# Kernel optimization log

Measured on AMD Instinct MI355X. Metric: run time of the kernel, lower is better.

Reference implementation:

```python
import jax, jax.numpy as jnp
import numpy as np
import math

B_, V_, D_, N_, H_, W_ = 4, 8, 64, 16, 32, 32
V_LIST = [0.0, 45.0, 90.0, 135.0, 180.0, 225.0, 270.0, 315.0]
GROUPS = 4
EPS = 1e-5


def _make_sample_coords():
    # Replicates F.affine_grid(align_corners=False) for fixed rotation matrices,
    # then maps normalized grid coords to input pixel coords as grid_sample does.
    xs = (np.arange(W_) + 0.5) * 2.0 / W_ - 1.0
    ys = (np.arange(H_) + 0.5) * 2.0 / H_ - 1.0
    X, Y = np.meshgrid(xs, ys)  # (H, W)
    ix_list, iy_list = [], []
    for w in V_LIST:
        a = math.radians(-w)
        c, s = math.cos(a), math.sin(a)
        gx = c * X - s * Y  # theta = [[c,-s,0],[s,c,0]]
        gy = s * X + c * Y
        ix_list.append((gx + 1.0) * W_ / 2.0 - 0.5)
        iy_list.append((gy + 1.0) * H_ / 2.0 - 0.5)
    return (jnp.asarray(np.stack(ix_list), jnp.float32),
            jnp.asarray(np.stack(iy_list), jnp.float32))

IX, IY = _make_sample_coords()  # each (V, H, W)


def _bilinear(sv, iy, ix):
    # sv: (B, D, N, H, W); iy, ix: (H, W) float sampling coords (pixel space)
    x0 = jnp.floor(ix)
    y0 = jnp.floor(iy)
    wx1 = ix - x0
    wy1 = iy - y0

    def corner(yc, xc, wgt):
        m = (yc >= 0) & (yc < H_) & (xc >= 0) & (xc < W_)  # zeros padding
        yi = jnp.clip(yc, 0, H_ - 1).astype(jnp.int32)
        xi = jnp.clip(xc, 0, W_ - 1).astype(jnp.int32)
        return sv[..., yi, xi] * jnp.where(m, wgt, 0.0)

    return (corner(y0, x0, (1.0 - wy1) * (1.0 - wx1))
            + corner(y0, x0 + 1.0, (1.0 - wy1) * wx1)
            + corner(y0 + 1.0, x0, wy1 * (1.0 - wx1))
            + corner(y0 + 1.0, x0 + 1.0, wy1 * wx1))

# vmap over the velocity axis V of s_prev and the per-velocity grids
_transport = jax.vmap(_bilinear, in_axes=(1, 0, 0), out_axes=1)


def _conv(x, w, b=None):
    y = jax.lax.conv_general_dilated(x, w, (1, 1), 'SAME',
                                     dimension_numbers=('NCHW', 'OIHW', 'NCHW'))
    if b is not None:
        y = y + b[None, :, None, None]
    return y


def _group_norm(x, w, b):
    Bn, D, H, W = x.shape
    xg = x.reshape(Bn, GROUPS, D // GROUPS, H, W)
    mu = xg.mean(axis=(2, 3, 4), keepdims=True)
    var = xg.var(axis=(2, 3, 4), keepdims=True)
    xn = ((xg - mu) * jax.lax.rsqrt(var + EPS)).reshape(Bn, D, H, W)
    return xn * w[None, :, None, None] + b[None, :, None, None]


def setup_inputs() -> dict:
    key = jax.random.key(0)
    ks = jax.random.split(key, 5)
    return {
        "u_t": jax.random.normal(ks[0], (B_, D_, H_, W_), jnp.float32),
        "s_prev": jax.random.normal(ks[1], (B_, V_, D_, N_, H_, W_), jnp.float32) * 0.1,
        "gn_w": jnp.ones((D_,), jnp.float32),
        "gn_b": jnp.zeros((D_,), jnp.float32),
        "conv_delta_w": jax.random.normal(ks[2], (D_, D_, 3, 3), jnp.float32) * 0.02,
        "conv_delta_b": jnp.zeros((D_,), jnp.float32),
        "conv_B_w": jax.random.normal(ks[3], (N_, D_, 3, 3), jnp.float32) * 0.02,
        "conv_C_w": jax.random.normal(ks[4], (N_, D_, 3, 3), jnp.float32) * 0.02,
        "log_A_real": jnp.full((D_, N_), math.log(0.5), jnp.float32),
        "D_param": jnp.ones((D_,), jnp.float32),
        "dt_bias": jnp.float32(math.log(math.e - 1.0)),
    }


def reference(u_t, s_prev, gn_w, gn_b, conv_delta_w, conv_delta_b,
              conv_B_w, conv_C_w, log_A_real, D_param, dt_bias):
    u_norm = _group_norm(u_t, gn_w, gn_b)
    delta = jax.nn.softplus(_conv(u_norm, conv_delta_w, conv_delta_b) + dt_bias)
    delta = jnp.clip(delta, 1e-4, 5.0)                               # (B,D,H,W)
    B_val = _conv(u_norm, conv_B_w)                                  # (B,N,H,W)
    C_val = _conv(u_norm, conv_C_w)                                  # (B,N,H,W)
    A = -jnp.exp(log_A_real)                                         # (D,N)
    A_bar = jnp.exp(delta[:, :, None] * A[None, :, :, None, None])   # (B,D,N,H,W)
    B_bar = delta[:, :, None] * B_val[:, None]                       # (B,D,N,H,W)
    s_trans = _transport(s_prev, IY, IX)                             # (B,V,D,N,H,W)
    s_new = A_bar[:, None] * s_trans + B_bar[:, None] * u_t[:, None, :, None]
    y_state = jnp.einsum('bvdnhw,bnhw->bvdhw', s_new, C_val)
    y_new = y_state + u_t[:, None] * D_param[None, None, :, None, None]
    return (y_new, s_new)
```

## Files before the change

kernel.cpp:

```cpp
#include <hip/hip_runtime.h>
#include <cmath>

#define FSQ 0.70710678118654752440f
__constant__ float CTAB[8] = {1.f,  FSQ, 0.f, -FSQ, -1.f, -FSQ, 0.f, FSQ};
__constant__ float STAB[8] = {0.f, -FSQ, -1.f, -FSQ,  0.f,  FSQ, 1.f, FSQ};

__global__ __launch_bounds__(256) void gn_kernel(const float* __restrict__ u,
                                                 const float* __restrict__ gw,
                                                 const float* __restrict__ gb,
                                                 float* __restrict__ up)
{
    int blk = blockIdx.x;
    int b = blk >> 2, g = blk & 3;
    int t = threadIdx.x;
    const float* src = u + ((size_t)(b * 64 + g * 16) << 10);
    float sum = 0.f, sq = 0.f;
    #pragma unroll
    for (int r = 0; r < 64; ++r) {
        float v = src[t + (r << 8)];
        sum += v; sq += v * v;
    }
    __shared__ float red[256], red2[256];
    red[t] = sum; red2[t] = sq;
    __syncthreads();
    for (int ofs = 128; ofs > 0; ofs >>= 1) {
        if (t < ofs) { red[t] += red[t + ofs]; red2[t] += red2[t + ofs]; }
        __syncthreads();
    }
    float mu  = red[0] * (1.f / 16384.f);
    float var = red2[0] * (1.f / 16384.f) - mu * mu;
    float rs  = rsqrtf(var + 1e-5f);

    float* pb = up + (size_t)(b * 64 + g * 16) * 1156;
    for (int k = t; k < 16 * 132; k += 256) {
        int pl = k / 132, c = k % 132;
        int idx;
        if (c < 34)       idx = c;
        else if (c < 68)  idx = 33 * 34 + (c - 34);
        else if (c < 100) idx = (c - 68 + 1) * 34;
        else              idx = (c - 100 + 1) * 34 + 33;
        pb[pl * 1156 + idx] = 0.f;
    }
    for (int r = 0; r < 64; ++r) {
        int idx = t + (r << 8);
        int ch = idx >> 10, rem = idx & 1023;
        int y = rem >> 5, x = rem & 31;
        float val = (src[idx] - mu) * rs * gw[g * 16 + ch] + gb[g * 16 + ch];
        pb[ch * 1156 + (y + 1) * 34 + (x + 1)] = val;
    }
}

__global__ __launch_bounds__(256) void conv_kernel(const float* __restrict__ up,
                                                   const float* __restrict__ wd,
                                                   const float* __restrict__ bd,
                                                   const float* __restrict__ wB,
                                                   const float* __restrict__ wC,
                                                   const float* __restrict__ dtb,
                                                   float* __restrict__ delta,
                                                   float* __restrict__ Bv,
                                                   float* __restrict__ Cv)
{
    __shared__ float sin_[64 * 204];
    __shared__ float red[256];
    int blk = blockIdx.x;
    int strip = blk & 7;
    int o = (blk >> 3) & 127; o = o % 96;
    o = ((blk >> 3) - (blk / 768) * 96);
    int b = blk / 768;
    int h0 = strip * 4;
    int t = threadIdx.x;

    const float* plane = up + (size_t)b * 73984;
    for (int idx = t; idx < 13056; idx += 256) {
        int ci = idx / 204;
        int rem = idx - ci * 204;
        sin_[idx] = plane[ci * 1156 + h0 * 34 + rem];
    }
    __syncthreads();

    const float* wsel;
    if (o < 64)      wsel = wd + (size_t)o * 576;
    else if (o < 80) wsel = wB + (size_t)(o - 64) * 576;
    else             wsel = wC + (size_t)(o - 80) * 576;

    int half = t >> 7;
    int px = t & 127;
    int r = px >> 5, c = px & 31;
    const float* base = sin_ + r * 34 + c;

    float acc = 0.f;
    int ci0 = half * 32;
    for (int ci = ci0; ci < ci0 + 32; ++ci) {
        const float* pp = base + ci * 204;
        const float* wp = wsel + ci * 9;
        #pragma unroll
        for (int dy = 0; dy < 3; ++dy)
            #pragma unroll
            for (int dx = 0; dx < 3; ++dx)
                acc += pp[dy * 34 + dx] * wp[dy * 3 + dx];
    }
    red[t] = acc;
    __syncthreads();
    if (t < 128) {
        float a = red[t] + red[t + 128];
        int pidx = (h0 + r) * 32 + c;
        if (o < 64) {
            float x = a + bd[o] + dtb[0];
            float sp = (x > 20.f) ? x : log1pf(expf(x));
            sp = fminf(fmaxf(sp, 1e-4f), 5.f);
            delta[((size_t)(b * 64 + o) << 10) + pidx] = sp;
        } else if (o < 80) {
            Bv[((size_t)(b * 16 + o - 64) << 10) + pidx] = a;
        } else {
            Cv[((size_t)(b * 16 + o - 80) << 10) + pidx] = a;
        }
    }
}

__global__ __launch_bounds__(256) void fused_state_kernel(
    const float* __restrict__ s_prev, const float* __restrict__ u_t,
    const float* __restrict__ delta, const float* __restrict__ Bv,
    const float* __restrict__ Cv, const float* __restrict__ logA,
    const float* __restrict__ Dp, float* __restrict__ y_out,
    float* __restrict__ s_out)
{
    __shared__ float lds[8 * 1156];
    __shared__ float Ash[8];
    int blk = blockIdx.x;
    int cchunk = blk & 1;
    int d = (blk >> 1) & 63, v = (blk >> 7) & 7, b = blk >> 10;
    int t = threadIdx.x;

    if (t < 8) Ash[t] = -__expf(logA[d * 16 + cchunk * 8 + t]);
    for (int k = t; k < 1056; k += 256) {
        int pl = k >> 7; int g = k & 127;
        pl = k / 132; g = k - pl * 132;
        int idx;
        if (g < 34)       idx = g;
        else if (g < 68)  idx = 1122 + (g - 34);
        else if (g < 100) idx = (g - 67) * 34;
        else              idx = (g - 99) * 34 + 33;
        lds[pl * 1156 + idx] = 0.f;
    }

    size_t so = (((size_t)((b * 8 + v) * 64 + d)) << 14) + (cchunk << 13);
    const float4* src = (const float4*)(s_prev + so);
    #pragma unroll
    for (int k = 0; k < 8; ++k) {
        int q = t + (k << 8);
        float4 val = src[q];
        int lin = q << 2;
        int nn = lin >> 10, rem = lin & 1023;
        int di = nn * 1156 + ((rem >> 5) + 1) * 34 + (rem & 31) + 1;
        lds[di] = val.x; lds[di + 1] = val.y; lds[di + 2] = val.z; lds[di + 3] = val.w;
    }
    __syncthreads();

    const float cc = CTAB[v], ss = STAB[v];
    const float* dpl = delta + ((size_t)(b * 64 + d) << 10);
    const float* upl = u_t   + ((size_t)(b * 64 + d) << 10);
    const float* bvc = Bv + ((size_t)b << 14) + (cchunk << 13);
    const float* cvc = Cv + ((size_t)b << 14) + (cchunk << 13);
    float* soc = s_out + so;
    float* yo  = y_out + (((size_t)((b * 8 + v) * 64 + d)) << 10);
    float Dd = Dp[d];

    for (int i = 0; i < 4; ++i) {
        int p = t + (i << 8);
        int h = p >> 5, wpx = p & 31;
        float X = (wpx + 0.5f) * 0.0625f - 1.f;
        float Y = (h + 0.5f) * 0.0625f - 1.f;
        float gx = cc * X - ss * Y;
        float gy = ss * X + cc * Y;
        float ix = (gx + 1.f) * 16.f - 0.5f;
        float iy = (gy + 1.f) * 16.f - 0.5f;
        float fx0 = floorf(ix), fy0 = floorf(iy);
        float wx = ix - fx0, wy = iy - fy0;
        int x0 = (int)fx0, y0 = (int)fy0;
        float mx0 = (x0 >= 0 && x0 < 32) ? (1.f - wx) : 0.f;
        float mx1 = (x0 >= -1 && x0 < 31) ? wx : 0.f;
        float my0 = (y0 >= 0 && y0 < 32) ? (1.f - wy) : 0.f;
        float my1 = (y0 >= -1 && y0 < 31) ? wy : 0.f;
        float w00 = my0 * mx0, w01 = my0 * mx1;
        float w10 = my1 * mx0, w11 = my1 * mx1;
        int bx = min(max(x0, -1), 31), by = min(max(y0, -1), 31);
        int base = (by + 1) * 34 + (bx + 1);

        float dd = dpl[p], uv = upl[p];
        float du = dd * uv;
        float yacc = 0.f;
        #pragma unroll
        for (int nn = 0; nn < 8; ++nn) {
            int si = base + nn * 1156;
            float s00 = lds[si], s01 = lds[si + 1];
            float s10 = lds[si + 34], s11 = lds[si + 35];
            float bil = s00 * w00 + s01 * w01 + s10 * w10 + s11 * w11;
            float abar = __expf(dd * Ash[nn]);
            float bvv = bvc[(nn << 10) + p];
            float sn = abar * bil + du * bvv;
            soc[(nn << 10) + p] = sn;
            yacc += sn * cvc[(nn << 10) + p];
        }
        float val = yacc + (cchunk == 0 ? uv * Dd : 0.f);
        atomicAdd(yo + p, val);
    }
}

extern "C" void kernel_launch(void* const* d_in, const int* in_sizes, int n_in,
                              void* d_out, int out_size, void* d_ws, size_t ws_size,
                              hipStream_t stream)
{
    const float* u_t    = (const float*)d_in[0];
    const float* s_prev = (const float*)d_in[1];
    const float* gn_w   = (const float*)d_in[2];
    const float* gn_b   = (const float*)d_in[3];
    const float* wd     = (const float*)d_in[4];
    const float* bd     = (const float*)d_in[5];
    const float* wB     = (const float*)d_in[6];
    const float* wC     = (const float*)d_in[7];
    const float* logA   = (const float*)d_in[8];
    const float* Dp     = (const float*)d_in[9];
    const float* dtb    = (const float*)d_in[10];

    float* y_out = (float*)d_out;
    float* s_out = y_out + 2097152;

    float* up    = (float*)d_ws;
    float* delta = up + 295936;
    float* Bv    = delta + 262144;
    float* Cv    = Bv + 65536;

    hipMemsetAsync(y_out, 0, (size_t)2097152 * sizeof(float), stream);

    hipLaunchKernelGGL(gn_kernel, dim3(16), dim3(256), 0, stream, u_t, gn_w, gn_b, up);
    hipLaunchKernelGGL(conv_kernel, dim3(3072), dim3(256), 0, stream,
                       up, wd, bd, wB, wC, dtb, delta, Bv, Cv);
    hipLaunchKernelGGL(fused_state_kernel, dim3(4096), dim3(256), 0, stream,
                       s_prev, u_t, delta, Bv, Cv, logA, Dp, y_out, s_out);
}
```

Measured before the change: 319.6 us.

## Compute four output channels per conv block and widen group-norm blocks

The conv kernel now computes four output channels per block. Each shared-memory input value is reused across four accumulators, and the grid shrinks from 3072 to 768 blocks, so input tiles are loaded from global memory a quarter as often. The group-norm kernel moves to 1024 threads per block with a wavefront shuffle reduction in place of the tree reduction through shared memory. In exchange, the conv kernel uses more registers and runs fewer blocks, which lowers parallelism.

```diff
diff --git a/kernel.cpp b/kernel.cpp
--- a/kernel.cpp
+++ b/kernel.cpp
@@ -5,10 +5,10 @@
 __constant__ float CTAB[8] = {1.f,  FSQ, 0.f, -FSQ, -1.f, -FSQ, 0.f, FSQ};
 __constant__ float STAB[8] = {0.f, -FSQ, -1.f, -FSQ,  0.f,  FSQ, 1.f, FSQ};
 
-__global__ __launch_bounds__(256) void gn_kernel(const float* __restrict__ u,
-                                                 const float* __restrict__ gw,
-                                                 const float* __restrict__ gb,
-                                                 float* __restrict__ up)
+__global__ __launch_bounds__(1024) void gn_kernel(const float* __restrict__ u,
+                                                  const float* __restrict__ gw,
+                                                  const float* __restrict__ gb,
+                                                  float* __restrict__ up)
 {
     int blk = blockIdx.x;
     int b = blk >> 2, g = blk & 3;
@@ -16,24 +16,29 @@
     const float* src = u + ((size_t)(b * 64 + g * 16) << 10);
     float sum = 0.f, sq = 0.f;
     #pragma unroll
-    for (int r = 0; r < 64; ++r) {
-        float v = src[t + (r << 8)];
+    for (int r = 0; r < 16; ++r) {
+        float v = src[t + (r << 10)];
         sum += v; sq += v * v;
     }
-    __shared__ float red[256], red2[256];
-    red[t] = sum; red2[t] = sq;
-    __syncthreads();
-    for (int ofs = 128; ofs > 0; ofs >>= 1) {
-        if (t < ofs) { red[t] += red[t + ofs]; red2[t] += red2[t + ofs]; }
-        __syncthreads();
-    }
-    float mu  = red[0] * (1.f / 16384.f);
-    float var = red2[0] * (1.f / 16384.f) - mu * mu;
+    #pragma unroll
+    for (int ofs = 32; ofs > 0; ofs >>= 1) {
+        sum += __shfl_down(sum, ofs);
+        sq  += __shfl_down(sq, ofs);
+    }
+    __shared__ float red[16], red2[16];
+    int wv = t >> 6;
+    if ((t & 63) == 0) { red[wv] = sum; red2[wv] = sq; }
+    __syncthreads();
+    float s_tot = 0.f, q_tot = 0.f;
+    #pragma unroll
+    for (int k = 0; k < 16; ++k) { s_tot += red[k]; q_tot += red2[k]; }
+    float mu  = s_tot * (1.f / 16384.f);
+    float var = q_tot * (1.f / 16384.f) - mu * mu;
     float rs  = rsqrtf(var + 1e-5f);
 
     float* pb = up + (size_t)(b * 64 + g * 16) * 1156;
-    for (int k = t; k < 16 * 132; k += 256) {
-        int pl = k / 132, c = k % 132;
+    for (int k = t; k < 16 * 132; k += 1024) {
+        int pl = k / 132, c = k - pl * 132;
         int idx;
         if (c < 34)       idx = c;
         else if (c < 68)  idx = 33 * 34 + (c - 34);
@@ -41,12 +46,11 @@
         else              idx = (c - 100 + 1) * 34 + 33;
         pb[pl * 1156 + idx] = 0.f;
     }
-    for (int r = 0; r < 64; ++r) {
-        int idx = t + (r << 8);
-        int ch = idx >> 10, rem = idx & 1023;
-        int y = rem >> 5, x = rem & 31;
-        float val = (src[idx] - mu) * rs * gw[g * 16 + ch] + gb[g * 16 + ch];
-        pb[ch * 1156 + (y + 1) * 34 + (x + 1)] = val;
+    int y = t >> 5, x = t & 31;
+    #pragma unroll
+    for (int r = 0; r < 16; ++r) {
+        float val = (src[t + (r << 10)] - mu) * rs * gw[g * 16 + r] + gb[g * 16 + r];
+        pb[r * 1156 + (y + 1) * 34 + (x + 1)] = val;
     }
 }
 
@@ -61,12 +65,10 @@
                                                    float* __restrict__ Cv)
 {
     __shared__ float sin_[64 * 204];
-    __shared__ float red[256];
     int blk = blockIdx.x;
     int strip = blk & 7;
-    int o = (blk >> 3) & 127; o = o % 96;
-    o = ((blk >> 3) - (blk / 768) * 96);
-    int b = blk / 768;
+    int og = (blk >> 3) % 24;
+    int b = blk / 192;
     int h0 = strip * 4;
     int t = threadIdx.x;
 
@@ -78,17 +80,18 @@
     }
     __syncthreads();
 
+    int o0 = og * 4;
     const float* wsel;
-    if (o < 64)      wsel = wd + (size_t)o * 576;
-    else if (o < 80) wsel = wB + (size_t)(o - 64) * 576;
-    else             wsel = wC + (size_t)(o - 80) * 576;
+    if (o0 < 64)      wsel = wd + (size_t)o0 * 576;
+    else if (o0 < 80) wsel = wB + (size_t)(o0 - 64) * 576;
+    else              wsel = wC + (size_t)(o0 - 80) * 576;
 
     int half = t >> 7;
     int px = t & 127;
     int r = px >> 5, c = px & 31;
     const float* base = sin_ + r * 34 + c;
 
-    float acc = 0.f;
+    float acc0 = 0.f, acc1 = 0.f, acc2 = 0.f, acc3 = 0.f;
     int ci0 = half * 32;
     for (int ci = ci0; ci < ci0 + 32; ++ci) {
         const float* pp = base + ci * 204;
@@ -96,23 +99,40 @@
         #pragma unroll
         for (int dy = 0; dy < 3; ++dy)
             #pragma unroll
-            for (int dx = 0; dx < 3; ++dx)
-                acc += pp[dy * 34 + dx] * wp[dy * 3 + dx];
-    }
-    red[t] = acc;
+            for (int dx = 0; dx < 3; ++dx) {
+                float v = pp[dy * 34 + dx];
+                int wi = dy * 3 + dx;
+                acc0 += v * wp[wi];
+                acc1 += v * wp[576 + wi];
+                acc2 += v * wp[1152 + wi];
+                acc3 += v * wp[1728 + wi];
+            }
+    }
+    __syncthreads();
+    float4* red4 = (float4*)sin_;
+    red4[t] = make_float4(acc0, acc1, acc2, acc3);
     __syncthreads();
     if (t < 128) {
-        float a = red[t] + red[t + 128];
+        float4 a = red4[t], bq = red4[t + 128];
+        float s0 = a.x + bq.x, s1 = a.y + bq.y, s2 = a.z + bq.z, s3 = a.w + bq.w;
+        float s[4] = {s0, s1, s2, s3};
         int pidx = (h0 + r) * 32 + c;
-        if (o < 64) {
-            float x = a + bd[o] + dtb[0];
-            float sp = (x > 20.f) ? x : log1pf(expf(x));
-            sp = fminf(fmaxf(sp, 1e-4f), 5.f);
-            delta[((size_t)(b * 64 + o) << 10) + pidx] = sp;
-        } else if (o < 80) {
-            Bv[((size_t)(b * 16 + o - 64) << 10) + pidx] = a;
+        if (o0 < 64) {
+            #pragma unroll
+            for (int k = 0; k < 4; ++k) {
+                float x = s[k] + bd[o0 + k] + dtb[0];
+                float sp = (x > 20.f) ? x : log1pf(expf(x));
+                sp = fminf(fmaxf(sp, 1e-4f), 5.f);
+                delta[((size_t)(b * 64 + o0 + k) << 10) + pidx] = sp;
+            }
+        } else if (o0 < 80) {
+            #pragma unroll
+            for (int k = 0; k < 4; ++k)
+                Bv[((size_t)(b * 16 + o0 - 64 + k) << 10) + pidx] = s[k];
         } else {
-            Cv[((size_t)(b * 16 + o - 80) << 10) + pidx] = a;
+            #pragma unroll
+            for (int k = 0; k < 4; ++k)
+                Cv[((size_t)(b * 16 + o0 - 80 + k) << 10) + pidx] = s[k];
         }
     }
 }
@@ -133,8 +153,7 @@
 
     if (t < 8) Ash[t] = -__expf(logA[d * 16 + cchunk * 8 + t]);
     for (int k = t; k < 1056; k += 256) {
-        int pl = k >> 7; int g = k & 127;
-        pl = k / 132; g = k - pl * 132;
+        int pl = k / 132, g = k - pl * 132;
         int idx;
         if (g < 34)       idx = g;
         else if (g < 68)  idx = 1122 + (g - 34);
@@ -232,8 +251,8 @@
 
     hipMemsetAsync(y_out, 0, (size_t)2097152 * sizeof(float), stream);
 
-    hipLaunchKernelGGL(gn_kernel, dim3(16), dim3(256), 0, stream, u_t, gn_w, gn_b, up);
-    hipLaunchKernelGGL(conv_kernel, dim3(3072), dim3(256), 0, stream,
+    hipLaunchKernelGGL(gn_kernel, dim3(16), dim3(1024), 0, stream, u_t, gn_w, gn_b, up);
+    hipLaunchKernelGGL(conv_kernel, dim3(768), dim3(256), 0, stream,
                        up, wd, bd, wB, wC, dtb, delta, Bv, Cv);
     hipLaunchKernelGGL(fused_state_kernel, dim3(4096), dim3(256), 0, stream,
                        s_prev, u_t, delta, Bv, Cv, logA, Dp, y_out, s_out);
```

Result: faster. 305.3 us (-4.5%).
